# Kernel optimization log

Measured on AMD Instinct MI355X. Metric: run time of the kernel, lower is better.

Reference implementation:

```python
import jax, jax.numpy as jnp
import numpy as np

D_MODEL = 1024
NUM_HEADS = 16
D_K = D_MODEL // NUM_HEADS
SCALE = 1.0 / np.sqrt(D_K).astype(np.float32)


def _rope_cos_sin(T, d_k):
    inv_freq = 1.0 / (10000.0 ** (jnp.arange(0, d_k, 2, dtype=jnp.float32) / d_k))
    t = jnp.arange(T, dtype=jnp.float32)
    freqs = jnp.outer(t, inv_freq)                      # [T, d_k/2]
    emb = jnp.concatenate([freqs, freqs], axis=-1)      # [T, d_k]
    return jnp.cos(emb)[None, None], jnp.sin(emb)[None, None]  # [1,1,T,d_k]


def _rotate_half(x):
    x1, x2 = x[..., : x.shape[-1] // 2], x[..., x.shape[-1] // 2 :]
    return jnp.concatenate([-x2, x1], axis=-1)


def setup_inputs() -> dict:
    key = jax.random.key(0)
    ks = jax.random.split(key, 8)
    B, T, C = 2, 2048, D_MODEL
    x = jax.random.normal(ks[0], (B, T, C), dtype=jnp.float32)
    # torch nn.Linear weights are [out, in]; forward does x @ W.T
    s = 1.0 / np.sqrt(C)
    Wq = jax.random.uniform(ks[1], (C, C), jnp.float32, -s, s)
    Wk = jax.random.uniform(ks[2], (C, C), jnp.float32, -s, s)
    Wv = jax.random.uniform(ks[3], (C, C), jnp.float32, -s, s)
    Wo = jax.random.uniform(ks[4], (C, C), jnp.float32, -s, s)
    bo = jax.random.uniform(ks[5], (C,), jnp.float32, -s, s)
    sector_bias = jnp.zeros((1, NUM_HEADS, 1, 1), dtype=jnp.float32)
    sector_weights = jax.random.uniform(ks[6], (B, T), jnp.float32, 0.5, 1.5)
    # causal mask, broadcastable to [B,H,T,T]; 0 -> masked
    mask = jnp.tril(jnp.ones((T, T), dtype=jnp.int32))[None, None]
    return {
        "x": x, "Wq": Wq, "Wk": Wk, "Wv": Wv, "Wo": Wo, "bo": bo,
        "sector_bias": sector_bias, "sector_weights": sector_weights,
        "mask": mask,
    }


def reference(x, Wq, Wk, Wv, Wo, bo, sector_bias, sector_weights, mask):
    B, T, C = x.shape
    H, dk = NUM_HEADS, D_K
    q = (x @ Wq.T).reshape(B, T, H, dk).transpose(0, 2, 1, 3)  # [B,H,T,dk]
    k = (x @ Wk.T).reshape(B, T, H, dk).transpose(0, 2, 1, 3)
    v = (x @ Wv.T).reshape(B, T, H, dk).transpose(0, 2, 1, 3)
    cos, sin = _rope_cos_sin(T, dk)
    q = q * cos + _rotate_half(q) * sin
    k = k * cos + _rotate_half(k) * sin
    scores = jnp.einsum("bhqd,bhkd->bhqk", q, k) * SCALE
    scores = scores + sector_bias
    scores = scores * sector_weights[:, None, None, :]  # broadcast over key dim
    scores = jnp.where(mask == 0, -jnp.inf, scores)
    attn = jax.nn.softmax(scores, axis=-1)
    out = jnp.einsum("bhqk,bhkd->bhqd", attn, v)
    out = out.transpose(0, 2, 1, 3).reshape(B, T, C)
    return out @ Wo.T + bo
```

## Files before the change

### kernel.cpp

```cpp
#include <hip/hip_runtime.h>


typedef __bf16 bf16x8 __attribute__((ext_vector_type(8)));
typedef float f32x4 __attribute__((ext_vector_type(4)));
typedef float f32x16 __attribute__((ext_vector_type(16)));
typedef unsigned short u16x8 __attribute__((ext_vector_type(8)));

__device__ __forceinline__ unsigned short f2bf(float f) {
    union { float f; unsigned int u; } c; c.f = f;
    unsigned int u = c.u;
    unsigned int r = u + 0x7fffu + ((u >> 16) & 1u);
    return (unsigned short)(r >> 16);
}
__device__ __forceinline__ unsigned cvtpk(float lo, float hi) {
    unsigned r;
    asm("v_cvt_pk_bf16_f32 %0, %1, %2" : "=v"(r) : "v"(lo), "v"(hi));
    return r;
}
__device__ __forceinline__ void plswap(unsigned a, unsigned b, unsigned& r0, unsigned& r1) {
#if __has_builtin(__builtin_amdgcn_permlane32_swap)
    auto s = __builtin_amdgcn_permlane32_swap(a, b, false, false);
    r0 = (unsigned)s[0]; r1 = (unsigned)s[1];
#else
    const int hh = (int)(threadIdx.x & 63) >> 5;
    const unsigned oa = (unsigned)__shfl_xor((int)a, 32);
    const unsigned ob = (unsigned)__shfl_xor((int)b, 32);
    r0 = hh ? ob : a;
    r1 = hh ? b : oa;
#endif
}
__device__ __forceinline__ void stage8_f32(unsigned short* dst, const float* src) {
    const float4 a = *(const float4*)src;
    const float4 b = *(const float4*)(src + 4);
    u16x8 v;
    v[0] = f2bf(a.x); v[1] = f2bf(a.y); v[2] = f2bf(a.z); v[3] = f2bf(a.w);
    v[4] = f2bf(b.x); v[5] = f2bf(b.y); v[6] = f2bf(b.z); v[7] = f2bf(b.w);
    *(u16x8*)dst = v;
}
__device__ __forceinline__ void async16(const unsigned short* g, unsigned short* l) {
    __builtin_amdgcn_global_load_lds(
        (const __attribute__((address_space(1))) void*)g,
        (__attribute__((address_space(3))) void*)l, 16, 0, 0);
}

__global__ __launch_bounds__(256) void cvt_all(
    const float* __restrict__ x, const float* __restrict__ Wq, const float* __restrict__ Wk,
    const float* __restrict__ Wv, const float* __restrict__ Wo,
    unsigned short* __restrict__ dst, int hasX, int n8)
{
    const int i = blockIdx.x * 256 + threadIdx.x;
    if (i >= n8) return;
    int r = i;
    const float* src; int off;
    const int xg = hasX ? 524288 : 0;
    if (r < xg) { src = x; off = r; }
    else {
        r -= xg;
        const int w = r >> 17, o = r & 131071;
        src = (w == 0) ? Wq : (w == 1) ? Wk : (w == 2) ? Wv : Wo;
        off = o;
    }
    stage8_f32(&dst[(size_t)i * 8], &src[(size_t)off * 8]);
}

template<int A_BF16>
__global__ __launch_bounds__(256) void gemm_qkv(
    const void* __restrict__ Av, const unsigned short* __restrict__ Wb,
    unsigned short* __restrict__ outv, const float* __restrict__ swg)
{
    constexpr int K = 1024, BK = 32;
    __shared__ __align__(16) unsigned short As[2][128 * BK];
    __shared__ __align__(16) unsigned short Bs[2][128 * BK];
    const int tid = threadIdx.x;
    const int wid = tid >> 6, lane = tid & 63, g = lane >> 4, l = lane & 15;
    const int wm = (wid & 1) * 64, wn = (wid >> 1) * 64;

    const int lin = blockIdx.x + (blockIdx.y << 3) + (blockIdx.z << 8);
    const int wg  = (lin & 7) * 96 + (lin >> 3);
    const int bx = wg & 7, by = (wg >> 3) & 31, bz = wg >> 8;
    const int m0 = by * 128, n0 = bx * 128;
    const int z = bz;
    const unsigned short* W = Wb + (size_t)z * 1048576;

    f32x4 acc[4][4];
#pragma unroll
    for (int i = 0; i < 4; ++i)
#pragma unroll
        for (int j = 0; j < 4; ++j) acc[i][j] = f32x4{0.f, 0.f, 0.f, 0.f};

    const int r = tid >> 2;
    const int c = (tid & 3) * 8;

    auto stage = [&](int buf, int k0) {
        if (A_BF16) {
            const unsigned short* A = (const unsigned short*)Av;
            unsigned short* AsW = &As[buf][wid * 512];
            async16(&A[(size_t)(m0 + r) * K + k0 + c], AsW);
            async16(&A[(size_t)(m0 + 64 + r) * K + k0 + c], AsW + 2048);
        } else {
            const float* A = (const float*)Av;
            stage8_f32(&As[buf][tid * 8],        &A[(size_t)(m0 + r) * K + k0 + c]);
            stage8_f32(&As[buf][tid * 8 + 2048], &A[(size_t)(m0 + 64 + r) * K + k0 + c]);
        }
        unsigned short* BsW = &Bs[buf][wid * 512];
        async16(&W[(size_t)(n0 + r) * K + k0 + c], BsW);
        async16(&W[(size_t)(n0 + 64 + r) * K + k0 + c], BsW + 2048);
    };

    stage(0, 0);
    __syncthreads();

    for (int k0 = 0; k0 < K; k0 += BK) {
        const int cur = (k0 >> 5) & 1;
        if (k0 + BK < K) stage(cur ^ 1, k0 + BK);

        const unsigned short* Asr = As[cur];
        const unsigned short* Bsr = Bs[cur];
        bf16x8 af[4], bfr[4];
#pragma unroll
        for (int im = 0; im < 4; ++im) af[im]  = *(const bf16x8*)&Asr[(wm + im * 16 + l) * BK + g * 8];
#pragma unroll
        for (int in = 0; in < 4; ++in) bfr[in] = *(const bf16x8*)&Bsr[(wn + in * 16 + l) * BK + g * 8];
#pragma unroll
        for (int im = 0; im < 4; ++im)
#pragma unroll
            for (int in = 0; in < 4; ++in)
                acc[im][in] = __builtin_amdgcn_mfma_f32_16x16x32_bf16(af[im], bfr[in], acc[im][in], 0, 0, 0);
        __syncthreads();
    }

    unsigned short* outq = outv + (size_t)z * 4194304;
    if (z < 2) {
        float freq[2];
#pragma unroll
        for (int in = 0; in < 2; ++in)
            freq[in] = exp2f(-(float)(in * 16 + l) * 0.41524101186f);
#pragma unroll
        for (int im = 0; im < 4; ++im)
#pragma unroll
            for (int i = 0; i < 4; ++i) {
                const int m = m0 + wm + im * 16 + g * 4 + i;
                const int b = m >> 11, t = m & 2047;
                float fw = 1.0f;
                if (z == 1) fw = 0.18033688011f * swg[(b << 11) + t];
#pragma unroll
                for (int in = 0; in < 2; ++in) {
                    const int n = n0 + wn + in * 16 + l;
                    const int h = n >> 6, d = n & 63;
                    const float ang = (float)t * freq[in];
                    const float cs = __cosf(ang), sn = __sinf(ang);
                    const float x1 = acc[im][in][i], x2 = acc[im][in + 2][i];
                    const size_t bidx = (((size_t)b * 16 + h) * 2048 + t) << 6;
                    outq[bidx + d]      = f2bf((x1 * cs - x2 * sn) * fw);
                    outq[bidx + d + 32] = f2bf((x2 * cs + x1 * sn) * fw);
                }
            }
    } else {
#pragma unroll
        for (int im = 0; im < 4; ++im)
#pragma unroll
            for (int in = 0; in < 4; ++in) {
                const int n = n0 + wn + in * 16 + l;
                const int h = n >> 6, d = n & 63;
                const int mb = m0 + wm + im * 16 + g * 4;
                const int bq = mb >> 11, t0 = mb & 2047;
                ushort4 pk;
                pk.x = f2bf(acc[im][in][0]); pk.y = f2bf(acc[im][in][1]);
                pk.z = f2bf(acc[im][in][2]); pk.w = f2bf(acc[im][in][3]);
                *(ushort4*)&outq[((size_t)(bq * 16 + h)) * 131072 + (size_t)d * 2048 + t0] = pk;
            }
    }
}

__global__ __launch_bounds__(256) void gemm_proj(
    const unsigned short* __restrict__ A, const unsigned short* __restrict__ W,
    float* __restrict__ out, const float* __restrict__ bias)
{
    constexpr int K = 1024, BK = 32;
    __shared__ __align__(16) unsigned short As[2][64 * BK];
    __shared__ __align__(16) unsigned short Bs[2][128 * BK];
    const int tid = threadIdx.x;
    const int wid = tid >> 6, lane = tid & 63, g = lane >> 4, l = lane & 15;
    const int wm = (wid & 1) * 32, wn = (wid >> 1) * 64;

    const int lin = blockIdx.x + (blockIdx.y << 3);
    const int wg  = (lin & 7) * 64 + (lin >> 3);
    const int m0 = (wg >> 3) * 64, n0 = (wg & 7) * 128;

    f32x4 acc[2][4];
#pragma unroll
    for (int i = 0; i < 2; ++i)
#pragma unroll
        for (int j = 0; j < 4; ++j) acc[i][j] = f32x4{0.f, 0.f, 0.f, 0.f};

    const int r = tid >> 2;
    const int c = (tid & 3) * 8;

    auto stage = [&](int buf, int k0) {
        unsigned short* AsW = &As[buf][wid * 512];
        unsigned short* BsW = &Bs[buf][wid * 512];
        async16(&A[(size_t)(m0 + r) * K + k0 + c], AsW);
        async16(&W[(size_t)(n0 + r) * K + k0 + c], BsW);
        async16(&W[(size_t)(n0 + 64 + r) * K + k0 + c], BsW + 2048);
    };

    stage(0, 0);
    __syncthreads();

    for (int k0 = 0; k0 < K; k0 += BK) {
        const int cur = (k0 >> 5) & 1;
        if (k0 + BK < K) stage(cur ^ 1, k0 + BK);

        const unsigned short* Asr = As[cur];
        const unsigned short* Bsr = Bs[cur];
        bf16x8 af[2], bfr[4];
#pragma unroll
        for (int im = 0; im < 2; ++im) af[im]  = *(const bf16x8*)&Asr[(wm + im * 16 + l) * BK + g * 8];
#pragma unroll
        for (int in = 0; in < 4; ++in) bfr[in] = *(const bf16x8*)&Bsr[(wn + in * 16 + l) * BK + g * 8];
#pragma unroll
        for (int im = 0; im < 2; ++im)
#pragma unroll
            for (int in = 0; in < 4; ++in)
                acc[im][in] = __builtin_amdgcn_mfma_f32_16x16x32_bf16(af[im], bfr[in], acc[im][in], 0, 0, 0);
        __syncthreads();
    }

#pragma unroll
    for (int im = 0; im < 2; ++im)
#pragma unroll
        for (int in = 0; in < 4; ++in) {
            const int n = n0 + wn + in * 16 + l;
#pragma unroll
            for (int i = 0; i < 4; ++i) {
                const int m = m0 + wm + im * 16 + g * 4 + i;
                out[(size_t)m * 1024 + n] = acc[im][in][i] + bias[n];
            }
        }
}

__global__ __launch_bounds__(128, 2) void flash_attn(
    const unsigned short* __restrict__ Q, const unsigned short* __restrict__ Kg,
    const unsigned short* __restrict__ VT, const float* __restrict__ sbias,
    const float* __restrict__ sw, unsigned short* __restrict__ attn)
{
    constexpr int T = 2048;
    __shared__ __align__(16) unsigned short Mem[64 * 72 * 2];
    unsigned short* Ks  = Mem;
    unsigned short* VsT = Mem + 64 * 72;
    float* Cmb = (float*)Mem;

    const int tid = threadIdx.x, wid = tid >> 6, lane = tid & 63;
    const int hl = lane & 31, hh = lane >> 5;
    const int id = blockIdx.x;
    const int p  = 63 - (id >> 5);
    const int bh = id & 31, b = bh >> 4, h = bh & 15;
    const size_t base = (size_t)bh * T * 64;
    const size_t vtb  = (size_t)bh * 64 * T;
    const float bias = sbias[h];
    const float* swb = sw + b * T;

    bf16x8 onef;
#pragma unroll
    for (int j = 0; j < 8; ++j) onef[j] = (__bf16)1.0f;

    const int q0 = p * 32;
    bf16x8 qf[4];
#pragma unroll
    for (int ks = 0; ks < 4; ++ks)
        qf[ks] = *(const bf16x8*)&Q[base + (size_t)(q0 + hl) * 64 + ks * 16 + hh * 8];

    f32x16 oacc[2], lrow;
#pragma unroll
    for (int r = 0; r < 16; ++r) { oacc[0][r] = 0.f; oacc[1][r] = 0.f; lrow[r] = 0.f; }

    u16x8 kpre[4], vpre[4];
#pragma unroll
    for (int s = 0; s < 4; ++s) {
        const int ci = s * 128 + tid, rr = ci >> 3, c8 = (ci & 7) * 8;
        kpre[s] = *(const u16x8*)&Kg[base + (size_t)rr * 64 + c8];
        vpre[s] = *(const u16x8*)&VT[vtb + (size_t)rr * T + c8];
    }

    const int rounds = (p + 2) >> 1;
    for (int rd = 0; rd < rounds; ++rd) {
        const int k0 = rd * 64;
        __syncthreads();
#pragma unroll
        for (int s = 0; s < 4; ++s) {
            const int ci = s * 128 + tid, rr = ci >> 3, c8 = (ci & 7) * 8;
            *(u16x8*)&Ks[rr * 72 + c8]  = kpre[s];
            *(u16x8*)&VsT[rr * 72 + c8] = vpre[s];
        }
        __syncthreads();
        if (rd + 1 < rounds) {
            const int k1 = k0 + 64;
#pragma unroll
            for (int s = 0; s < 4; ++s) {
                const int ci = s * 128 + tid, rr = ci >> 3, c8 = (ci & 7) * 8;
                kpre[s] = *(const u16x8*)&Kg[base + (size_t)(k1 + rr) * 64 + c8];
                vpre[s] = *(const u16x8*)&VT[vtb + (size_t)rr * T + k1 + c8];
            }
        }

        const int kw0 = k0 + wid * 32;
        if (kw0 <= q0 + 31) {
            f32x16 sx;
#pragma unroll
            for (int r = 0; r < 16; ++r) sx[r] = 0.f;
#pragma unroll
            for (int ks = 0; ks < 4; ++ks) {
                const bf16x8 kf = *(const bf16x8*)&Ks[(wid * 32 + hl) * 72 + ks * 16 + hh * 8];
                sx = __builtin_amdgcn_mfma_f32_32x32x16_bf16(kf, qf[ks], sx, 0, 0, 0);
            }
            if (bias != 0.0f) {
                const float bn = bias * 1.44269504f;
#pragma unroll
                for (int r = 0; r < 16; ++r) {
                    const int kl = (r & 3) + 8 * (r >> 2) + 4 * hh;
                    sx[r] += bn * swb[kw0 + kl];
                }
            }
            if (kw0 + 31 > q0) {
                const int dq = q0 + hl - kw0;
#pragma unroll
                for (int r = 0; r < 16; ++r) {
                    const int kl = (r & 3) + 8 * (r >> 2) + 4 * hh;
                    sx[r] = (kl <= dq) ? sx[r] : -1e30f;
                }
            }
#pragma unroll
            for (int r = 0; r < 16; ++r) sx[r] = exp2f(sx[r]);

            unsigned wds[8];
#pragma unroll
            for (int g2 = 0; g2 < 4; ++g2) {
                wds[g2 * 2]     = cvtpk(sx[g2 * 4],     sx[g2 * 4 + 1]);
                wds[g2 * 2 + 1] = cvtpk(sx[g2 * 4 + 2], sx[g2 * 4 + 3]);
            }
            bf16x8 pf[2];
#pragma unroll
            for (int ks = 0; ks < 2; ++ks) {
                unsigned a0, a1, b0, b1;
                plswap(wds[4 * ks],     wds[4 * ks + 2], a0, a1);
                plswap(wds[4 * ks + 1], wds[4 * ks + 3], b0, b1);
                union { unsigned u[4]; bf16x8 v; } pk_;
                pk_.u[0] = a0; pk_.u[1] = b0;
                pk_.u[2] = a1; pk_.u[3] = b1;
                pf[ks] = pk_.v;
            }

            lrow = __builtin_amdgcn_mfma_f32_32x32x16_bf16(pf[0], onef, lrow, 0, 0, 0);
            lrow = __builtin_amdgcn_mfma_f32_32x32x16_bf16(pf[1], onef, lrow, 0, 0, 0);

#pragma unroll
            for (int ks = 0; ks < 2; ++ks)
#pragma unroll
                for (int dt = 0; dt < 2; ++dt) {
                    const bf16x8 vf = *(const bf16x8*)&VsT[(dt * 32 + hl) * 72 + wid * 32 + ks * 16 + hh * 8];
                    oacc[dt] = __builtin_amdgcn_mfma_f32_32x32x16_bf16(pf[ks], vf, oacc[dt], 0, 0, 0);
                }
        }
    }

    __syncthreads();
    if (wid == 1) {
#pragma unroll
        for (int dt = 0; dt < 2; ++dt)
#pragma unroll
            for (int r = 0; r < 16; ++r) Cmb[(dt * 16 + r) * 64 + lane] = oacc[dt][r];
#pragma unroll
        for (int r = 0; r < 16; ++r) Cmb[2048 + r * 64 + lane] = lrow[r];
    }
    __syncthreads();
    if (wid == 0) {
#pragma unroll
        for (int r = 0; r < 16; ++r) {
            const float li = 1.0f / (lrow[r] + Cmb[2048 + r * 64 + lane]);
            const int row = (r & 3) + 8 * (r >> 2) + 4 * hh;
            const int qr = q0 + row;
#pragma unroll
            for (int dt = 0; dt < 2; ++dt) {
                const float ov = oacc[dt][r] + Cmb[(dt * 16 + r) * 64 + lane];
                attn[(size_t)(b * T + qr) * 1024 + h * 64 + dt * 32 + hl] = f2bf(ov * li);
            }
        }
    }
}

extern "C" void kernel_launch(void* const* d_in, const int* in_sizes, int n_in,
                              void* d_out, int out_size, void* d_ws, size_t ws_size,
                              hipStream_t stream) {
    const float* x  = (const float*)d_in[0];
    const float* Wq = (const float*)d_in[1];
    const float* Wk = (const float*)d_in[2];
    const float* Wv = (const float*)d_in[3];
    const float* Wo = (const float*)d_in[4];
    const float* bo = (const float*)d_in[5];
    const float* sb = (const float*)d_in[6];
    const float* sw = (const float*)d_in[7];

    const size_t QKV_SZ = 4194304;
    const size_t W_SZ   = 1048576;
    unsigned short* ws16 = (unsigned short*)d_ws;
    const bool big = ws_size >= 2 * (4 * QKV_SZ + 4 * W_SZ);

    if (big) {
        unsigned short* xb    = ws16;
        unsigned short* Wb3   = xb + QKV_SZ;
        unsigned short* Wob   = Wb3 + 3 * W_SZ;
        unsigned short* qkv   = Wob + W_SZ;
        unsigned short* attnb = xb;

        cvt_all<<<4096, 256, 0, stream>>>(x, Wq, Wk, Wv, Wo, xb, 1, 1048576);
        gemm_qkv<1><<<dim3(8, 32, 3), 256, 0, stream>>>(xb, Wb3, qkv, sw);
        flash_attn<<<2048, 128, 0, stream>>>(qkv, qkv + QKV_SZ, qkv + 2 * QKV_SZ,
                                             sb, sw, attnb);
        gemm_proj<<<dim3(8, 64), 256, 0, stream>>>(attnb, Wob, (float*)d_out, bo);
    } else {
        unsigned short* qkv   = ws16;
        unsigned short* attnb = qkv + 3 * QKV_SZ;
        unsigned short* Wb3   = attnb;
        unsigned short* Wob   = qkv;

        cvt_all<<<1536, 256, 0, stream>>>(x, Wq, Wk, Wv, Wo, Wb3, 0, 393216);
        gemm_qkv<0><<<dim3(8, 32, 3), 256, 0, stream>>>(x, Wb3, qkv, sw);
        flash_attn<<<2048, 128, 0, stream>>>(qkv, qkv + QKV_SZ, qkv + 2 * QKV_SZ,
                                             sb, sw, attnb);
        cvt_all<<<512, 256, 0, stream>>>(x, Wo, Wo, Wo, Wo, Wob, 0, 131072);
        gemm_proj<<<dim3(8, 64), 256, 0, stream>>>(attnb, Wob, (float*)d_out, bo);
    }
}
```

Before: 198.5 us.

## Store Q/K/V in MFMA-fragment order and load attention operands directly from global

The QKV projection epilogue now writes Q, K and V in a pre-swizzled layout that matches the per-lane MFMA operand fragments for 32-key chunks. Flash attention then drops the LDS staging of K/V tiles, the double-buffered register prefetch and the per-round barriers. Each wave reads its K and V fragments straight from global memory with contiguous 16-byte per-lane loads, and the two waves interleave over 32-key chunks. This removes LDS traffic and synchronisation, but gives up explicit prefetch, so global load latency is exposed unless occupancy or the compiler hides it. The K/V reuse across the two waves that LDS provided is also lost.

```diff
diff --git a/kernel.cpp b/kernel.cpp
--- a/kernel.cpp
+++ b/kernel.cpp
@@ -131,6 +131,7 @@
 
     unsigned short* outq = outv + (size_t)z * 4194304;
     if (z < 2) {
+        const int hq = (n0 + wn) >> 6;
         float freq[2];
 #pragma unroll
         for (int in = 0; in < 2; ++in)
@@ -143,16 +144,16 @@
                 const int b = m >> 11, t = m & 2047;
                 float fw = 1.0f;
                 if (z == 1) fw = 0.18033688011f * swg[(b << 11) + t];
+                const size_t fq = (size_t)((b << 4) + hq) * 131072
+                                + (size_t)((t >> 5) << 2) * 512
+                                + (size_t)((((l >> 3) & 1) << 5) + (t & 31)) * 8 + (l & 7);
 #pragma unroll
                 for (int in = 0; in < 2; ++in) {
-                    const int n = n0 + wn + in * 16 + l;
-                    const int h = n >> 6, d = n & 63;
                     const float ang = (float)t * freq[in];
                     const float cs = __cosf(ang), sn = __sinf(ang);
                     const float x1 = acc[im][in][i], x2 = acc[im][in + 2][i];
-                    const size_t bidx = (((size_t)b * 16 + h) * 2048 + t) << 6;
-                    outq[bidx + d]      = f2bf((x1 * cs - x2 * sn) * fw);
-                    outq[bidx + d + 32] = f2bf((x2 * cs + x1 * sn) * fw);
+                    outq[fq + (size_t)in * 512]       = f2bf((x1 * cs - x2 * sn) * fw);
+                    outq[fq + (size_t)(in + 2) * 512] = f2bf((x2 * cs + x1 * sn) * fw);
                 }
             }
     } else {
@@ -167,7 +168,10 @@
                 ushort4 pk;
                 pk.x = f2bf(acc[im][in][0]); pk.y = f2bf(acc[im][in][1]);
                 pk.z = f2bf(acc[im][in][2]); pk.w = f2bf(acc[im][in][3]);
-                *(ushort4*)&outq[((size_t)(bq * 16 + h)) * 131072 + (size_t)d * 2048 + t0] = pk;
+                const size_t fv = (size_t)((bq << 4) + h) * 131072
+                                + (size_t)(((t0 >> 5) << 2) + ((d >> 5) << 1) + ((t0 >> 4) & 1)) * 512
+                                + (size_t)((((t0 >> 3) & 1) << 5) + (d & 31)) * 8 + (t0 & 7);
+                *(ushort4*)&outq[fv] = pk;
             }
     }
 }
@@ -240,23 +244,19 @@
 }
 
 __global__ __launch_bounds__(128, 2) void flash_attn(
-    const unsigned short* __restrict__ Q, const unsigned short* __restrict__ Kg,
-    const unsigned short* __restrict__ VT, const float* __restrict__ sbias,
+    const unsigned short* __restrict__ Qf, const unsigned short* __restrict__ Kf,
+    const unsigned short* __restrict__ Vf, const float* __restrict__ sbias,
     const float* __restrict__ sw, unsigned short* __restrict__ attn)
 {
     constexpr int T = 2048;
-    __shared__ __align__(16) unsigned short Mem[64 * 72 * 2];
-    unsigned short* Ks  = Mem;
-    unsigned short* VsT = Mem + 64 * 72;
-    float* Cmb = (float*)Mem;
+    __shared__ float Cmb[3072];
 
     const int tid = threadIdx.x, wid = tid >> 6, lane = tid & 63;
     const int hl = lane & 31, hh = lane >> 5;
     const int id = blockIdx.x;
     const int p  = 63 - (id >> 5);
     const int bh = id & 31, b = bh >> 4, h = bh & 15;
-    const size_t base = (size_t)bh * T * 64;
-    const size_t vtb  = (size_t)bh * 64 * T;
+    const size_t fb = (size_t)bh * 131072;
     const float bias = sbias[h];
     const float* swb = sw + b * T;
 
@@ -268,99 +268,76 @@
     bf16x8 qf[4];
 #pragma unroll
     for (int ks = 0; ks < 4; ++ks)
-        qf[ks] = *(const bf16x8*)&Q[base + (size_t)(q0 + hl) * 64 + ks * 16 + hh * 8];
+        qf[ks] = *(const bf16x8*)&Qf[fb + (size_t)(p * 4 + ks) * 512 + lane * 8];
 
     f32x16 oacc[2], lrow;
 #pragma unroll
     for (int r = 0; r < 16; ++r) { oacc[0][r] = 0.f; oacc[1][r] = 0.f; lrow[r] = 0.f; }
 
-    u16x8 kpre[4], vpre[4];
-#pragma unroll
-    for (int s = 0; s < 4; ++s) {
-        const int ci = s * 128 + tid, rr = ci >> 3, c8 = (ci & 7) * 8;
-        kpre[s] = *(const u16x8*)&Kg[base + (size_t)rr * 64 + c8];
-        vpre[s] = *(const u16x8*)&VT[vtb + (size_t)rr * T + c8];
-    }
-
-    const int rounds = (p + 2) >> 1;
-    for (int rd = 0; rd < rounds; ++rd) {
-        const int k0 = rd * 64;
-        __syncthreads();
-#pragma unroll
-        for (int s = 0; s < 4; ++s) {
-            const int ci = s * 128 + tid, rr = ci >> 3, c8 = (ci & 7) * 8;
-            *(u16x8*)&Ks[rr * 72 + c8]  = kpre[s];
-            *(u16x8*)&VsT[rr * 72 + c8] = vpre[s];
-        }
-        __syncthreads();
-        if (rd + 1 < rounds) {
-            const int k1 = k0 + 64;
-#pragma unroll
-            for (int s = 0; s < 4; ++s) {
-                const int ci = s * 128 + tid, rr = ci >> 3, c8 = (ci & 7) * 8;
-                kpre[s] = *(const u16x8*)&Kg[base + (size_t)(k1 + rr) * 64 + c8];
-                vpre[s] = *(const u16x8*)&VT[vtb + (size_t)rr * T + k1 + c8];
-            }
-        }
-
-        const int kw0 = k0 + wid * 32;
-        if (kw0 <= q0 + 31) {
-            f32x16 sx;
-#pragma unroll
-            for (int r = 0; r < 16; ++r) sx[r] = 0.f;
-#pragma unroll
-            for (int ks = 0; ks < 4; ++ks) {
-                const bf16x8 kf = *(const bf16x8*)&Ks[(wid * 32 + hl) * 72 + ks * 16 + hh * 8];
-                sx = __builtin_amdgcn_mfma_f32_32x32x16_bf16(kf, qf[ks], sx, 0, 0, 0);
-            }
-            if (bias != 0.0f) {
-                const float bn = bias * 1.44269504f;
-#pragma unroll
-                for (int r = 0; r < 16; ++r) {
-                    const int kl = (r & 3) + 8 * (r >> 2) + 4 * hh;
-                    sx[r] += bn * swb[kw0 + kl];
-                }
-            }
-            if (kw0 + 31 > q0) {
-                const int dq = q0 + hl - kw0;
-#pragma unroll
-                for (int r = 0; r < 16; ++r) {
-                    const int kl = (r & 3) + 8 * (r >> 2) + 4 * hh;
-                    sx[r] = (kl <= dq) ? sx[r] : -1e30f;
-                }
-            }
-#pragma unroll
-            for (int r = 0; r < 16; ++r) sx[r] = exp2f(sx[r]);
-
-            unsigned wds[8];
-#pragma unroll
-            for (int g2 = 0; g2 < 4; ++g2) {
-                wds[g2 * 2]     = cvtpk(sx[g2 * 4],     sx[g2 * 4 + 1]);
-                wds[g2 * 2 + 1] = cvtpk(sx[g2 * 4 + 2], sx[g2 * 4 + 3]);
-            }
-            bf16x8 pf[2];
-#pragma unroll
-            for (int ks = 0; ks < 2; ++ks) {
-                unsigned a0, a1, b0, b1;
-                plswap(wds[4 * ks],     wds[4 * ks + 2], a0, a1);
-                plswap(wds[4 * ks + 1], wds[4 * ks + 3], b0, b1);
-                union { unsigned u[4]; bf16x8 v; } pk_;
-                pk_.u[0] = a0; pk_.u[1] = b0;
-                pk_.u[2] = a1; pk_.u[3] = b1;
-                pf[ks] = pk_.v;
-            }
-
-            lrow = __builtin_amdgcn_mfma_f32_32x32x16_bf16(pf[0], onef, lrow, 0, 0, 0);
-            lrow = __builtin_amdgcn_mfma_f32_32x32x16_bf16(pf[1], onef, lrow, 0, 0, 0);
-
-#pragma unroll
-            for (int ks = 0; ks < 2; ++ks)
-#pragma unroll
-                for (int dt = 0; dt < 2; ++dt) {
-                    const bf16x8 vf = *(const bf16x8*)&VsT[(dt * 32 + hl) * 72 + wid * 32 + ks * 16 + hh * 8];
-                    oacc[dt] = __builtin_amdgcn_mfma_f32_32x32x16_bf16(pf[ks], vf, oacc[dt], 0, 0, 0);
-                }
-        }
+    for (int c = wid; c <= p; c += 2) {
+        const unsigned short* kb = &Kf[fb + (size_t)c * 2048 + lane * 8];
+        const unsigned short* vb = &Vf[fb + (size_t)c * 2048 + lane * 8];
+
+        const bf16x8 kf0 = *(const bf16x8*)&kb[0];
+        const bf16x8 kf1 = *(const bf16x8*)&kb[512];
+        const bf16x8 kf2 = *(const bf16x8*)&kb[1024];
+        const bf16x8 kf3 = *(const bf16x8*)&kb[1536];
+        f32x16 sx;
+#pragma unroll
+        for (int r = 0; r < 16; ++r) sx[r] = 0.f;
+        sx = __builtin_amdgcn_mfma_f32_32x32x16_bf16(kf0, qf[0], sx, 0, 0, 0);
+        sx = __builtin_amdgcn_mfma_f32_32x32x16_bf16(kf1, qf[1], sx, 0, 0, 0);
+        sx = __builtin_amdgcn_mfma_f32_32x32x16_bf16(kf2, qf[2], sx, 0, 0, 0);
+        sx = __builtin_amdgcn_mfma_f32_32x32x16_bf16(kf3, qf[3], sx, 0, 0, 0);
+
+        const bf16x8 vf00 = *(const bf16x8*)&vb[0];
+        const bf16x8 vf01 = *(const bf16x8*)&vb[512];
+        const bf16x8 vf10 = *(const bf16x8*)&vb[1024];
+        const bf16x8 vf11 = *(const bf16x8*)&vb[1536];
+
+        if (bias != 0.0f) {
+            const float bn = bias * 1.44269504f;
+#pragma unroll
+            for (int r = 0; r < 16; ++r) {
+                const int kl = (r & 3) + 8 * (r >> 2) + 4 * hh;
+                sx[r] += bn * swb[c * 32 + kl];
+            }
+        }
+        if (c == p) {
+#pragma unroll
+            for (int r = 0; r < 16; ++r) {
+                const int kl = (r & 3) + 8 * (r >> 2) + 4 * hh;
+                sx[r] = (kl <= hl) ? sx[r] : -1e30f;
+            }
+        }
+#pragma unroll
+        for (int r = 0; r < 16; ++r) sx[r] = exp2f(sx[r]);
+
+        unsigned wds[8];
+#pragma unroll
+        for (int g2 = 0; g2 < 4; ++g2) {
+            wds[g2 * 2]     = cvtpk(sx[g2 * 4],     sx[g2 * 4 + 1]);
+            wds[g2 * 2 + 1] = cvtpk(sx[g2 * 4 + 2], sx[g2 * 4 + 3]);
+        }
+        bf16x8 pf[2];
+#pragma unroll
+        for (int ks = 0; ks < 2; ++ks) {
+            unsigned a0, a1, b0, b1;
+            plswap(wds[4 * ks],     wds[4 * ks + 2], a0, a1);
+            plswap(wds[4 * ks + 1], wds[4 * ks + 3], b0, b1);
+            union { unsigned u[4]; bf16x8 v; } pk_;
+            pk_.u[0] = a0; pk_.u[1] = b0;
+            pk_.u[2] = a1; pk_.u[3] = b1;
+            pf[ks] = pk_.v;
+        }
+
+        lrow = __builtin_amdgcn_mfma_f32_32x32x16_bf16(pf[0], onef, lrow, 0, 0, 0);
+        lrow = __builtin_amdgcn_mfma_f32_32x32x16_bf16(pf[1], onef, lrow, 0, 0, 0);
+
+        oacc[0] = __builtin_amdgcn_mfma_f32_32x32x16_bf16(pf[0], vf00, oacc[0], 0, 0, 0);
+        oacc[0] = __builtin_amdgcn_mfma_f32_32x32x16_bf16(pf[1], vf01, oacc[0], 0, 0, 0);
+        oacc[1] = __builtin_amdgcn_mfma_f32_32x32x16_bf16(pf[0], vf10, oacc[1], 0, 0, 0);
+        oacc[1] = __builtin_amdgcn_mfma_f32_32x32x16_bf16(pf[1], vf11, oacc[1], 0, 0, 0);
     }
 
     __syncthreads();
```

New measurement: 194.5 us. 1.02x faster.
